# Kernel optimization log

Measured on AMD Instinct MI355X. Metric: run time of the kernel, lower is better.

The kernel has to match this reference:

```python
import jax, jax.numpy as jnp
import numpy as np

IN_DIM = 32000   # source vocab
OUT_DIM = 32000  # target vocab
H = 1024         # hidden_dim
B = 32           # batch
SRC_LEN = 64     # encoder sequence length
MAX_LEN = 64     # decode steps
BOS = 1
NEG = jnp.float32(-1e9)


def setup_inputs() -> dict:
    key = jax.random.key(0)
    ks = jax.random.split(key, 12)
    s = jnp.float32(0.02)
    nrm = lambda k, shape: jax.random.normal(k, shape, jnp.float32) * s
    source = jax.random.randint(ks[0], (B, SRC_LEN), 1, IN_DIM, dtype=jnp.int32)
    return {
        "source": source,
        "emb_enc": nrm(ks[1], (IN_DIM, H)),
        "Wx_e": nrm(ks[2], (H, 4 * H)),
        "Wh_e": nrm(ks[3], (H, 4 * H)),
        "b_e": jnp.zeros((4 * H,), jnp.float32),
        "emb_dec": nrm(ks[4], (OUT_DIM, H)),
        "Wx_d": nrm(ks[5], (H, 4 * H)),
        "Wh_d": nrm(ks[6], (H, 4 * H)),
        "b_d": jnp.zeros((4 * H,), jnp.float32),
        "W_a": nrm(ks[7], (H, H)),
        "W_c": nrm(ks[8], (2 * H, H)),
        "b_c": jnp.zeros((H,), jnp.float32),
        "W_out": nrm(ks[9], (H, OUT_DIM)),
        "b_out": jnp.zeros((OUT_DIM,), jnp.float32),
    }


def lstm_cell(x, h, c, Wx, Wh, b):
    # Keras gate order: i, f, g(candidate), o
    z = x @ Wx + h @ Wh + b  # (B, 4H)
    i, f, g, o = jnp.split(z, 4, axis=-1)
    c2 = jax.nn.sigmoid(f) * c + jax.nn.sigmoid(i) * jnp.tanh(g)
    h2 = jax.nn.sigmoid(o) * jnp.tanh(c2)
    return h2, c2


def reference(source, emb_enc, Wx_e, Wh_e, b_e, emb_dec, Wx_d, Wh_d, b_d,
              W_a, W_c, b_c, W_out, b_out):
    # ---- Encoder LSTM over source ----
    x_src = emb_enc[source]                     # (B, S, H)
    h0 = jnp.zeros((B, H), jnp.float32)
    c0 = jnp.zeros((B, H), jnp.float32)

    def enc_step(carry, xt):
        h, c = carry
        h2, c2 = lstm_cell(xt, h, c, Wx_e, Wh_e, b_e)
        return (h2, c2), h2

    (h, c), hs = jax.lax.scan(enc_step, (h0, c0), jnp.swapaxes(x_src, 0, 1))
    hs = jnp.swapaxes(hs, 0, 1)                 # (B, S, H) encoder outputs

    # Precompute hs @ W_a once (attention key projection)
    hs_a = jnp.einsum('bsh,hk->bsk', hs, W_a)
    src_mask = source != 0                      # (B, S)

    y0 = jnp.full((B,), BOS, jnp.int32)

    def dec_step(carry, _):
        y, h, c = carry
        xt = emb_dec[y]                         # (B, H)
        h2, c2 = lstm_cell(xt, h, c, Wx_d, Wh_d, b_d)
        # mask_zero on decoder embedding: token 0 carries state/output
        m = (y != 0)[:, None]
        h2 = jnp.where(m, h2, h)
        c2 = jnp.where(m, c2, c)
        # Luong-style attention: score = ht . (hs W_a)
        score = jnp.einsum('bk,bsk->bs', h2, hs_a)
        score = jnp.where(src_mask, score, NEG)
        a = jax.nn.softmax(score, axis=-1)
        ctx = jnp.einsum('bs,bsh->bh', a, hs)
        ht = jnp.tanh(jnp.concatenate([ctx, h2], axis=-1) @ W_c + b_c)
        probs = jax.nn.softmax(ht @ W_out + b_out, axis=-1)  # (B, V)
        y_next = jnp.argmax(probs, axis=-1).astype(jnp.int32)
        return (y_next, h2, c2), probs

    _, out = jax.lax.scan(dec_step, (y0, h, c), None, length=MAX_LEN)
    return jnp.swapaxes(out, 0, 1)              # (B, MAX_LEN, OUT_DIM)
```

## Files before the change

kernel.cpp:

```cpp
#include <hip/hip_runtime.h>
#include <math.h>

#define BB 32
#define SS 64
#define HH 1024
#define VV 32000
#define NSTEPS 64

__device__ __forceinline__ float sigmoidf_(float x) { return 1.0f / (1.0f + expf(-x)); }

__global__ void init_hc(float* __restrict__ h, float* __restrict__ c) {
    int i = blockIdx.x * 256 + threadIdx.x;
    if (i < BB * HH) { h[i] = 0.f; c[i] = 0.f; }
}

template <int KS>
__global__ __launch_bounds__(256) void gemm_skinny(
    const float* __restrict__ A1, const float* __restrict__ A2,
    const int* __restrict__ tok, int tok_stride, const float* __restrict__ emb,
    const float* __restrict__ W1, const float* __restrict__ W2, int KW1,
    int N, int jblocks, float* __restrict__ outp)
{
    __shared__ alignas(16) float At[KS][36];
    const int tid = threadIdx.x;
    const int jb = blockIdx.x % jblocks;
    const int ks = blockIdx.x / jblocks;
    const int k0 = ks * KS;

    for (int i = tid; i < KS * BB; i += 256) {
        int b = i / KS;
        int k = i % KS;
        int kg = k0 + k;
        float v;
        if (kg < 1024) {
            const float* r = A1 ? (A1 + (size_t)b * 1024)
                                : (emb + (size_t)tok[b * tok_stride] * 1024);
            v = r[kg];
        } else {
            v = A2[(size_t)b * 1024 + (kg - 1024)];
        }
        At[k][b] = v;
    }
    __syncthreads();

    const int jj = jb * 256 + tid;
    if (2 * jj >= N) return;
    const float* Wbase = (k0 < KW1) ? (W1 + (size_t)k0 * N)
                                    : (W2 + (size_t)(k0 - KW1) * N);
    float2 acc[BB];
#pragma unroll
    for (int b = 0; b < BB; b++) { acc[b].x = 0.f; acc[b].y = 0.f; }

#pragma unroll 1
    for (int k = 0; k < KS; k++) {
        const float2 w = *(const float2*)(Wbase + (size_t)k * N + 2 * jj);
#pragma unroll
        for (int b = 0; b < BB; b += 4) {
            const float4 a = *(const float4*)&At[k][b];
            acc[b + 0].x = fmaf(a.x, w.x, acc[b + 0].x); acc[b + 0].y = fmaf(a.x, w.y, acc[b + 0].y);
            acc[b + 1].x = fmaf(a.y, w.x, acc[b + 1].x); acc[b + 1].y = fmaf(a.y, w.y, acc[b + 1].y);
            acc[b + 2].x = fmaf(a.z, w.x, acc[b + 2].x); acc[b + 2].y = fmaf(a.z, w.y, acc[b + 2].y);
            acc[b + 3].x = fmaf(a.w, w.x, acc[b + 3].x); acc[b + 3].y = fmaf(a.w, w.y, acc[b + 3].y);
        }
    }
#pragma unroll
    for (int b = 0; b < BB; b++) {
        *(float2*)(outp + ((size_t)ks * BB + b) * N + 2 * jj) = acc[b];
    }
}

__global__ __launch_bounds__(256) void enc_gates(
    const float* __restrict__ zpart, int nslices, const float* __restrict__ bias,
    float* __restrict__ h, float* __restrict__ c, float* __restrict__ hs, int s)
{
    int idx = blockIdx.x * 256 + threadIdx.x;
    int b = idx >> 10, j = idx & 1023;
    float zi = bias[j], zf = bias[1024 + j], zg = bias[2048 + j], zo = bias[3072 + j];
    for (int ks = 0; ks < nslices; ks++) {
        const float* zp = zpart + ((size_t)ks * BB + b) * 4096;
        zi += zp[j]; zf += zp[1024 + j]; zg += zp[2048 + j]; zo += zp[3072 + j];
    }
    float cp = c[idx];
    float c2 = sigmoidf_(zf) * cp + sigmoidf_(zi) * tanhf(zg);
    float h2 = sigmoidf_(zo) * tanhf(c2);
    c[idx] = c2; h[idx] = h2;
    hs[((size_t)b * SS + s) * HH + j] = h2;
}

__global__ __launch_bounds__(256) void hsa_kernel(
    const float* __restrict__ hs, const float* __restrict__ W_a,
    float* __restrict__ hs_a, int* __restrict__ y)
{
    if (blockIdx.x == 0 && threadIdx.x < BB) y[threadIdx.x] = 1;
    __shared__ alignas(16) float At[64][12];
    const int tid = threadIdx.x;
    const int rg = blockIdx.x & 255;
    const int jpb = blockIdx.x >> 8;
    const int jj = jpb * 256 + tid;
    float2 acc[8];
#pragma unroll
    for (int r = 0; r < 8; r++) { acc[r].x = 0.f; acc[r].y = 0.f; }

    for (int kc = 0; kc < 1024; kc += 64) {
        __syncthreads();
        for (int i = tid; i < 512; i += 256) {
            int r = i >> 6, k = i & 63;
            At[k][r] = hs[(size_t)(rg * 8 + r) * 1024 + kc + k];
        }
        __syncthreads();
#pragma unroll 1
        for (int k = 0; k < 64; k++) {
            float2 w = *(const float2*)(W_a + (size_t)(kc + k) * 1024 + 2 * jj);
            float4 a0 = *(const float4*)&At[k][0];
            float4 a1 = *(const float4*)&At[k][4];
            acc[0].x = fmaf(a0.x, w.x, acc[0].x); acc[0].y = fmaf(a0.x, w.y, acc[0].y);
            acc[1].x = fmaf(a0.y, w.x, acc[1].x); acc[1].y = fmaf(a0.y, w.y, acc[1].y);
            acc[2].x = fmaf(a0.z, w.x, acc[2].x); acc[2].y = fmaf(a0.z, w.y, acc[2].y);
            acc[3].x = fmaf(a0.w, w.x, acc[3].x); acc[3].y = fmaf(a0.w, w.y, acc[3].y);
            acc[4].x = fmaf(a1.x, w.x, acc[4].x); acc[4].y = fmaf(a1.x, w.y, acc[4].y);
            acc[5].x = fmaf(a1.y, w.x, acc[5].x); acc[5].y = fmaf(a1.y, w.y, acc[5].y);
            acc[6].x = fmaf(a1.z, w.x, acc[6].x); acc[6].y = fmaf(a1.z, w.y, acc[6].y);
            acc[7].x = fmaf(a1.w, w.x, acc[7].x); acc[7].y = fmaf(a1.w, w.y, acc[7].y);
        }
    }
#pragma unroll
    for (int r = 0; r < 8; r++)
        *(float2*)(hs_a + (size_t)(rg * 8 + r) * 1024 + 2 * jj) = acc[r];
}

__global__ __launch_bounds__(256) void attn_gates(
    const float* __restrict__ zpart, int nslices, const float* __restrict__ bias,
    const int* __restrict__ y, float* __restrict__ h, float* __restrict__ c,
    const float* __restrict__ hs_a, const float* __restrict__ hs,
    const int* __restrict__ source, float* __restrict__ ctx)
{
    __shared__ alignas(16) float h2s[HH];
    __shared__ float red[256];
    __shared__ float av[SS];
    const int b = blockIdx.x, tid = threadIdx.x;
    const bool m = (y[b] != 0);

    for (int u = 0; u < 4; u++) {
        int j = tid + 256 * u;
        float zi = bias[j], zf = bias[1024 + j], zg = bias[2048 + j], zo = bias[3072 + j];
        for (int ks = 0; ks < nslices; ks++) {
            const float* zp = zpart + ((size_t)ks * BB + b) * 4096;
            zi += zp[j]; zf += zp[1024 + j]; zg += zp[2048 + j]; zo += zp[3072 + j];
        }
        int idx = b * HH + j;
        float cp = c[idx], hp = h[idx];
        float c2 = sigmoidf_(zf) * cp + sigmoidf_(zi) * tanhf(zg);
        float h2 = sigmoidf_(zo) * tanhf(c2);
        if (!m) { c2 = cp; h2 = hp; }
        c[idx] = c2; h[idx] = h2; h2s[j] = h2;
    }
    __syncthreads();

    {
        int t = tid & 63, kc = tid >> 6;
        const float4* row = (const float4*)(hs_a + ((size_t)b * SS + t) * HH) + kc * 64;
        const float4* hv = (const float4*)h2s + kc * 64;
        float sc = 0.f;
#pragma unroll 4
        for (int i = 0; i < 64; i++) {
            float4 a = row[i], x = hv[i];
            sc += a.x * x.x + a.y * x.y + a.z * x.z + a.w * x.w;
        }
        red[tid] = sc;
    }
    __syncthreads();
    if (tid < 64) {
        float s = red[tid] + red[tid + 64] + red[tid + 128] + red[tid + 192];
        if (source[b * SS + tid] == 0) s = -1e9f;
        red[tid] = s;
    }
    __syncthreads();
    if (tid < 64) {
        float mx = -3.4e38f;
        for (int i = 0; i < 64; i++) mx = fmaxf(mx, red[i]);
        av[tid] = expf(red[tid] - mx);
    }
    __syncthreads();
    if (tid < 64) {
        float ssum = 0.f;
        for (int i = 0; i < 64; i++) ssum += av[i];
        av[tid] = av[tid] / ssum;
    }
    __syncthreads();
    for (int u = 0; u < 4; u++) {
        int j = tid + 256 * u;
        float s = 0.f;
        for (int t = 0; t < SS; t++) s += av[t] * hs[((size_t)b * SS + t) * HH + j];
        ctx[b * HH + j] = s;
    }
}

__global__ __launch_bounds__(256) void ht_reduce(
    const float* __restrict__ wcpart, int nslices,
    const float* __restrict__ b_c, float* __restrict__ ht)
{
    int idx = blockIdx.x * 256 + threadIdx.x;
    int b = idx >> 10, j = idx & 1023;
    float s = b_c[j];
    for (int ks = 0; ks < nslices; ks++) s += wcpart[((size_t)ks * BB + b) * HH + j];
    ht[idx] = tanhf(s);
}

__global__ __launch_bounds__(256) void softmax_out(
    const float* __restrict__ lpart,
    const float* __restrict__ b_out, float* __restrict__ lrow,
    float* __restrict__ out, int* __restrict__ y, int step)
{
    __shared__ float rv[256];
    __shared__ int ri[256];
    __shared__ float rs[256];
    const int b = blockIdx.x, tid = threadIdx.x;
    float bmax = -3.4e38f; int barg = 0;
    for (int v = tid; v < VV; v += 256) {
        float l = b_out[v];
        l += lpart[((size_t)0 * BB + b) * VV + v];
        l += lpart[((size_t)1 * BB + b) * VV + v];
        l += lpart[((size_t)2 * BB + b) * VV + v];
        l += lpart[((size_t)3 * BB + b) * VV + v];
        lrow[(size_t)b * VV + v] = l;
        if (l > bmax) { bmax = l; barg = v; }
    }
    rv[tid] = bmax; ri[tid] = barg;
    __syncthreads();
    for (int off = 128; off > 0; off >>= 1) {
        if (tid < off) {
            float v2 = rv[tid + off]; int i2 = ri[tid + off];
            if (v2 > rv[tid] || (v2 == rv[tid] && i2 < ri[tid])) { rv[tid] = v2; ri[tid] = i2; }
        }
        __syncthreads();
    }
    const float mx = rv[0];
    float ls = 0.f;
    for (int v = tid; v < VV; v += 256) ls += expf(lrow[(size_t)b * VV + v] - mx);
    rs[tid] = ls;
    __syncthreads();
    for (int off = 128; off > 0; off >>= 1) {
        if (tid < off) rs[tid] += rs[tid + off];
        __syncthreads();
    }
    const float inv = 1.0f / rs[0];
    float* orow = out + ((size_t)b * NSTEPS + step) * VV;
    for (int v = tid; v < VV; v += 256) orow[v] = expf(lrow[(size_t)b * VV + v] - mx) * inv;
    if (tid == 0) y[b] = ri[0];
}

extern "C" void kernel_launch(void* const* d_in, const int* in_sizes, int n_in,
                              void* d_out, int out_size, void* d_ws, size_t ws_size,
                              hipStream_t stream)
{
    const int*   source  = (const int*)d_in[0];
    const float* emb_enc = (const float*)d_in[1];
    const float* Wx_e    = (const float*)d_in[2];
    const float* Wh_e    = (const float*)d_in[3];
    const float* b_e     = (const float*)d_in[4];
    const float* emb_dec = (const float*)d_in[5];
    const float* Wx_d    = (const float*)d_in[6];
    const float* Wh_d    = (const float*)d_in[7];
    const float* b_d     = (const float*)d_in[8];
    const float* W_a     = (const float*)d_in[9];
    const float* W_c     = (const float*)d_in[10];
    const float* b_c     = (const float*)d_in[11];
    const float* W_out   = (const float*)d_in[12];
    const float* b_out   = (const float*)d_in[13];
    float* out = (float*)d_out;

    float* ws = (float*)d_ws;
    float* h    = ws;
    float* c    = h + 32768;
    float* hs   = c + 32768;
    float* hs_a = hs + 2097152;
    float* ctxb = hs_a + 2097152;
    float* htb  = ctxb + 32768;
    float* zpart  = htb + 32768;
    float* wcpart = zpart + 4194304;
    int*   y = (int*)(wcpart + 2097152);
    float* lpart = zpart;
    float* lrow  = wcpart;

    init_hc<<<128, 256, 0, stream>>>(h, c);

    for (int s = 0; s < SS; s++) {
        gemm_skinny<64><<<256, 256, 0, stream>>>(
            nullptr, h, source + s, SS, emb_enc, Wx_e, Wh_e, 1024, 4096, 8, zpart);
        enc_gates<<<128, 256, 0, stream>>>(zpart, 32, b_e, h, c, hs, s);
    }

    hsa_kernel<<<512, 256, 0, stream>>>(hs, W_a, hs_a, y);

    for (int t = 0; t < NSTEPS; t++) {
        gemm_skinny<64><<<256, 256, 0, stream>>>(
            nullptr, h, y, 1, emb_dec, Wx_d, Wh_d, 1024, 4096, 8, zpart);
        attn_gates<<<32, 256, 0, stream>>>(zpart, 32, b_d, y, h, c, hs_a, hs, source, ctxb);
        gemm_skinny<32><<<128, 256, 0, stream>>>(
            ctxb, h, nullptr, 0, nullptr, W_c, nullptr, 2048, 1024, 2, wcpart);
        ht_reduce<<<128, 256, 0, stream>>>(wcpart, 64, b_c, htb);
        gemm_skinny<256><<<252, 256, 0, stream>>>(
            htb, nullptr, nullptr, 0, nullptr, W_out, nullptr, 1024, 32000, 63, lpart);
        softmax_out<<<32, 256, 0, stream>>>(lpart, b_out, lrow, out, y, t);
    }
}
```

Before: 25.53 ms.

## Fuse encoder and decoder loops into one cooperative persistent megakernel

```diff
diff --git a/kernel.cpp b/kernel.cpp
--- a/kernel.cpp
+++ b/kernel.cpp
@@ -1,13 +1,293 @@
 #include <hip/hip_runtime.h>
+#include <hip/hip_cooperative_groups.h>
 #include <math.h>
+
+namespace cg = cooperative_groups;
 
 #define BB 32
 #define SS 64
 #define HH 1024
 #define VV 32000
 #define NSTEPS 64
+#define GRID 256
 
 __device__ __forceinline__ float sigmoidf_(float x) { return 1.0f / (1.0f + expf(-x)); }
+
+
+struct MegaP {
+    const int* source; const float* emb_enc;
+    const float* Wx_e; const float* Wh_e; const float* b_e;
+    const float* emb_dec; const float* Wx_d; const float* Wh_d; const float* b_d;
+    const float* W_a; const float* W_c; const float* b_c;
+    const float* W_out; const float* b_out;
+    float* out;
+    float* h; float* c; float* hs; float* hs_a; float* ctx; float* ht;
+    float* zpart; float* wcpart; int* y;
+};
+
+union SharedU {
+    float At[256][36];
+    float hsaAt[64][12];
+    struct { float h2s[HH]; float red[256]; float av[SS]; } a;
+    struct { float rv[256]; int ri[256]; float rs[256]; } s;
+};
+
+template <int KS>
+__device__ void gemm_tile(
+    const float* __restrict__ A1, const float* __restrict__ A2,
+    const int* __restrict__ tok, int tok_stride, const float* __restrict__ emb,
+    const float* __restrict__ W1, const float* __restrict__ W2, int KW1,
+    int N, int jblocks, int tile, float* __restrict__ outp, float (*At)[36])
+{
+    const int tid = threadIdx.x;
+    const int jb = tile % jblocks;
+    const int ks = tile / jblocks;
+    const int k0 = ks * KS;
+
+    __syncthreads();
+    for (int i = tid; i < KS * BB; i += 256) {
+        int b = i / KS;
+        int k = i % KS;
+        int kg = k0 + k;
+        float v;
+        if (kg < 1024) {
+            const float* r = A1 ? (A1 + (size_t)b * 1024)
+                                : (emb + (size_t)tok[b * tok_stride] * 1024);
+            v = r[kg];
+        } else {
+            v = A2[(size_t)b * 1024 + (kg - 1024)];
+        }
+        At[k][b] = v;
+    }
+    __syncthreads();
+
+    const int jj = jb * 256 + tid;
+    if (2 * jj < N) {
+        const float* Wbase = (k0 < KW1) ? (W1 + (size_t)k0 * N)
+                                        : (W2 + (size_t)(k0 - KW1) * N);
+        float2 acc[BB];
+#pragma unroll
+        for (int b = 0; b < BB; b++) { acc[b].x = 0.f; acc[b].y = 0.f; }
+
+#pragma unroll 4
+        for (int k = 0; k < KS; k++) {
+            const float2 w = *(const float2*)(Wbase + (size_t)k * N + 2 * jj);
+#pragma unroll
+            for (int b = 0; b < BB; b += 4) {
+                const float4 a = *(const float4*)&At[k][b];
+                acc[b + 0].x = fmaf(a.x, w.x, acc[b + 0].x); acc[b + 0].y = fmaf(a.x, w.y, acc[b + 0].y);
+                acc[b + 1].x = fmaf(a.y, w.x, acc[b + 1].x); acc[b + 1].y = fmaf(a.y, w.y, acc[b + 1].y);
+                acc[b + 2].x = fmaf(a.z, w.x, acc[b + 2].x); acc[b + 2].y = fmaf(a.z, w.y, acc[b + 2].y);
+                acc[b + 3].x = fmaf(a.w, w.x, acc[b + 3].x); acc[b + 3].y = fmaf(a.w, w.y, acc[b + 3].y);
+            }
+        }
+#pragma unroll
+        for (int b = 0; b < BB; b++) {
+            *(float2*)(outp + ((size_t)ks * BB + b) * N + 2 * jj) = acc[b];
+        }
+    }
+}
+
+__device__ void hsa_tile(const float* __restrict__ hs, const float* __restrict__ W_a,
+                         float* __restrict__ hs_a, int tile, float (*At)[12])
+{
+    const int tid = threadIdx.x;
+    const int rg = tile & 255;
+    const int jpb = tile >> 8;
+    const int jj = jpb * 256 + tid;
+    float2 acc[8];
+#pragma unroll
+    for (int r = 0; r < 8; r++) { acc[r].x = 0.f; acc[r].y = 0.f; }
+
+    for (int kc = 0; kc < 1024; kc += 64) {
+        __syncthreads();
+        for (int i = tid; i < 512; i += 256) {
+            int r = i >> 6, k = i & 63;
+            At[k][r] = hs[(size_t)(rg * 8 + r) * 1024 + kc + k];
+        }
+        __syncthreads();
+#pragma unroll 1
+        for (int k = 0; k < 64; k++) {
+            float2 w = *(const float2*)(W_a + (size_t)(kc + k) * 1024 + 2 * jj);
+            float4 a0 = *(const float4*)&At[k][0];
+            float4 a1 = *(const float4*)&At[k][4];
+            acc[0].x = fmaf(a0.x, w.x, acc[0].x); acc[0].y = fmaf(a0.x, w.y, acc[0].y);
+            acc[1].x = fmaf(a0.y, w.x, acc[1].x); acc[1].y = fmaf(a0.y, w.y, acc[1].y);
+            acc[2].x = fmaf(a0.z, w.x, acc[2].x); acc[2].y = fmaf(a0.z, w.y, acc[2].y);
+            acc[3].x = fmaf(a0.w, w.x, acc[3].x); acc[3].y = fmaf(a0.w, w.y, acc[3].y);
+            acc[4].x = fmaf(a1.x, w.x, acc[4].x); acc[4].y = fmaf(a1.x, w.y, acc[4].y);
+            acc[5].x = fmaf(a1.y, w.x, acc[5].x); acc[5].y = fmaf(a1.y, w.y, acc[5].y);
+            acc[6].x = fmaf(a1.z, w.x, acc[6].x); acc[6].y = fmaf(a1.z, w.y, acc[6].y);
+            acc[7].x = fmaf(a1.w, w.x, acc[7].x); acc[7].y = fmaf(a1.w, w.y, acc[7].y);
+        }
+    }
+#pragma unroll
+    for (int r = 0; r < 8; r++)
+        *(float2*)(hs_a + (size_t)(rg * 8 + r) * 1024 + 2 * jj) = acc[r];
+}
+
+__device__ void attn_phase(const MegaP& p, int b, SharedU& sh)
+{
+    const int tid = threadIdx.x;
+    const bool m = (p.y[b] != 0);
+
+    for (int u = 0; u < 4; u++) {
+        int j = tid + 256 * u;
+        float zi = p.b_d[j], zf = p.b_d[1024 + j], zg = p.b_d[2048 + j], zo = p.b_d[3072 + j];
+        for (int ks = 0; ks < 32; ks++) {
+            const float* zp = p.zpart + ((size_t)ks * BB + b) * 4096;
+            zi += zp[j]; zf += zp[1024 + j]; zg += zp[2048 + j]; zo += zp[3072 + j];
+        }
+        int idx = b * HH + j;
+        float cp = p.c[idx], hp = p.h[idx];
+        float c2 = sigmoidf_(zf) * cp + sigmoidf_(zi) * tanhf(zg);
+        float h2 = sigmoidf_(zo) * tanhf(c2);
+        if (!m) { c2 = cp; h2 = hp; }
+        p.c[idx] = c2; p.h[idx] = h2; sh.a.h2s[j] = h2;
+    }
+    __syncthreads();
+
+    {
+        int t = tid & 63, kc = tid >> 6;
+        const float4* row = (const float4*)(p.hs_a + ((size_t)b * SS + t) * HH) + kc * 64;
+        const float4* hv = (const float4*)sh.a.h2s + kc * 64;
+        float sc = 0.f;
+#pragma unroll 4
+        for (int i = 0; i < 64; i++) {
+            float4 a = row[i], x = hv[i];
+            sc += a.x * x.x + a.y * x.y + a.z * x.z + a.w * x.w;
+        }
+        sh.a.red[tid] = sc;
+    }
+    __syncthreads();
+    if (tid < 64) {
+        float s = sh.a.red[tid] + sh.a.red[tid + 64] + sh.a.red[tid + 128] + sh.a.red[tid + 192];
+        if (p.source[b * SS + tid] == 0) s = -1e9f;
+        sh.a.red[tid] = s;
+    }
+    __syncthreads();
+    if (tid < 64) {
+        float mx = -3.4e38f;
+        for (int i = 0; i < 64; i++) mx = fmaxf(mx, sh.a.red[i]);
+        sh.a.av[tid] = expf(sh.a.red[tid] - mx);
+    }
+    __syncthreads();
+    if (tid < 64) {
+        float ssum = 0.f;
+        for (int i = 0; i < 64; i++) ssum += sh.a.av[i];
+        sh.a.av[tid] = sh.a.av[tid] / ssum;
+    }
+    __syncthreads();
+    for (int u = 0; u < 4; u++) {
+        int j = tid + 256 * u;
+        float s = 0.f;
+        for (int t2 = 0; t2 < SS; t2++) s += sh.a.av[t2] * p.hs[((size_t)b * SS + t2) * HH + j];
+        p.ctx[b * HH + j] = s;
+    }
+}
+
+__device__ void softmax_phase(const MegaP& p, int b, int step, SharedU& sh)
+{
+    const int tid = threadIdx.x;
+    const float* lpart = p.zpart;
+    float* lrow = p.wcpart;
+
+    float bmax = -3.4e38f; int barg = 0;
+    for (int v = tid; v < VV; v += 256) {
+        float l = p.b_out[v];
+        l += lpart[((size_t)0 * BB + b) * VV + v];
+        l += lpart[((size_t)1 * BB + b) * VV + v];
+        l += lpart[((size_t)2 * BB + b) * VV + v];
+        l += lpart[((size_t)3 * BB + b) * VV + v];
+        lrow[(size_t)b * VV + v] = l;
+        if (l > bmax) { bmax = l; barg = v; }
+    }
+    sh.s.rv[tid] = bmax; sh.s.ri[tid] = barg;
+    __syncthreads();
+    for (int off = 128; off > 0; off >>= 1) {
+        if (tid < off) {
+            float v2 = sh.s.rv[tid + off]; int i2 = sh.s.ri[tid + off];
+            if (v2 > sh.s.rv[tid] || (v2 == sh.s.rv[tid] && i2 < sh.s.ri[tid])) {
+                sh.s.rv[tid] = v2; sh.s.ri[tid] = i2;
+            }
+        }
+        __syncthreads();
+    }
+    const float mx = sh.s.rv[0];
+    float ls = 0.f;
+    for (int v = tid; v < VV; v += 256) ls += expf(lrow[(size_t)b * VV + v] - mx);
+    sh.s.rs[tid] = ls;
+    __syncthreads();
+    for (int off = 128; off > 0; off >>= 1) {
+        if (tid < off) sh.s.rs[tid] += sh.s.rs[tid + off];
+        __syncthreads();
+    }
+    const float inv = 1.0f / sh.s.rs[0];
+    float* orow = p.out + ((size_t)b * NSTEPS + step) * VV;
+    for (int v = tid; v < VV; v += 256) orow[v] = expf(lrow[(size_t)b * VV + v] - mx) * inv;
+    if (tid == 0) p.y[b] = sh.s.ri[0];
+}
+
+__global__ __launch_bounds__(256) void mega(MegaP p)
+{
+    cg::grid_group grid = cg::this_grid();
+    __shared__ SharedU sh;
+    const int bid = blockIdx.x;
+    const int tid = threadIdx.x;
+    const int gidx = bid * 256 + tid;
+
+    if (gidx < BB * HH) { p.h[gidx] = 0.f; p.c[gidx] = 0.f; }
+    if (gidx < BB) p.y[gidx] = 1;
+    grid.sync();
+
+    for (int s = 0; s < SS; s++) {
+        gemm_tile<64>(nullptr, p.h, p.source + s, SS, p.emb_enc,
+                      p.Wx_e, p.Wh_e, 1024, 4096, 8, bid, p.zpart, sh.At);
+        grid.sync();
+        if (gidx < BB * HH) {
+            int b = gidx >> 10, j = gidx & 1023;
+            float zi = p.b_e[j], zf = p.b_e[1024 + j], zg = p.b_e[2048 + j], zo = p.b_e[3072 + j];
+            for (int ks = 0; ks < 32; ks++) {
+                const float* zp = p.zpart + ((size_t)ks * BB + b) * 4096;
+                zi += zp[j]; zf += zp[1024 + j]; zg += zp[2048 + j]; zo += zp[3072 + j];
+            }
+            float cp = p.c[gidx];
+            float c2 = sigmoidf_(zf) * cp + sigmoidf_(zi) * tanhf(zg);
+            float h2 = sigmoidf_(zo) * tanhf(c2);
+            p.c[gidx] = c2; p.h[gidx] = h2;
+            p.hs[((size_t)b * SS + s) * HH + j] = h2;
+        }
+        grid.sync();
+    }
+
+    for (int tile = bid; tile < 512; tile += GRID)
+        hsa_tile(p.hs, p.W_a, p.hs_a, tile, sh.hsaAt);
+    grid.sync();
+
+    for (int t = 0; t < NSTEPS; t++) {
+        gemm_tile<64>(nullptr, p.h, p.y, 1, p.emb_dec,
+                      p.Wx_d, p.Wh_d, 1024, 4096, 8, bid, p.zpart, sh.At);
+        grid.sync();
+        if (bid < BB) attn_phase(p, bid, sh);
+        grid.sync();
+        if (bid < 128) gemm_tile<32>(p.ctx, p.h, nullptr, 0, nullptr,
+                                     p.W_c, nullptr, 2048, 1024, 2, bid, p.wcpart, sh.At);
+        grid.sync();
+        if (gidx < BB * HH) {
+            int b = gidx >> 10, j = gidx & 1023;
+            float sum = p.b_c[j];
+            for (int ks = 0; ks < 64; ks++) sum += p.wcpart[((size_t)ks * BB + b) * HH + j];
+            p.ht[gidx] = tanhf(sum);
+        }
+        grid.sync();
+        if (bid < 252) gemm_tile<256>(p.ht, nullptr, nullptr, 0, nullptr,
+                                      p.W_out, nullptr, 1024, 32000, 63, bid, p.zpart, sh.At);
+        grid.sync();
+        if (bid < BB) softmax_phase(p, bid, t, sh);
+        grid.sync();
+    }
+}
+
 
 __global__ void init_hc(float* __restrict__ h, float* __restrict__ c) {
     int i = blockIdx.x * 256 + threadIdx.x;
@@ -282,16 +562,28 @@
     float* lpart = zpart;
     float* lrow  = wcpart;
 
+    MegaP pr;
+    pr.source = source; pr.emb_enc = emb_enc;
+    pr.Wx_e = Wx_e; pr.Wh_e = Wh_e; pr.b_e = b_e;
+    pr.emb_dec = emb_dec; pr.Wx_d = Wx_d; pr.Wh_d = Wh_d; pr.b_d = b_d;
+    pr.W_a = W_a; pr.W_c = W_c; pr.b_c = b_c;
+    pr.W_out = W_out; pr.b_out = b_out;
+    pr.out = out;
+    pr.h = h; pr.c = c; pr.hs = hs; pr.hs_a = hs_a; pr.ctx = ctxb; pr.ht = htb;
+    pr.zpart = zpart; pr.wcpart = wcpart; pr.y = y;
+
+    void* args[] = { &pr };
+    hipError_t err = hipLaunchCooperativeKernel(mega, dim3(GRID), dim3(256),
+                                                args, 0u, stream);
+    if (err == hipSuccess) return;
+
     init_hc<<<128, 256, 0, stream>>>(h, c);
-
     for (int s = 0; s < SS; s++) {
         gemm_skinny<64><<<256, 256, 0, stream>>>(
             nullptr, h, source + s, SS, emb_enc, Wx_e, Wh_e, 1024, 4096, 8, zpart);
         enc_gates<<<128, 256, 0, stream>>>(zpart, 32, b_e, h, c, hs, s);
     }
-
     hsa_kernel<<<512, 256, 0, stream>>>(hs, W_a, hs_a, y);
-
     for (int t = 0; t < NSTEPS; t++) {
         gemm_skinny<64><<<256, 256, 0, stream>>>(
             nullptr, h, y, 1, emb_dec, Wx_d, Wh_d, 1024, 4096, 8, zpart);
```

Measured after the change: 54.96 ms. +115.3%, slower.
